# Performance work log

Hardware: AMD Instinct MI355X
Metric: run time of the kernel (lower is better)

The kernel has to match this reference:

```python
import jax, jax.numpy as jnp
import numpy as np

D, V, B, T = 512, 32000, 64, 32


def setup_inputs() -> dict:
    key = jax.random.key(0)
    ks = jax.random.split(key, 12)
    s = 1.0 / np.sqrt(D)
    u = lambda k, shape: jax.random.uniform(k, shape, jnp.float32, -s, s)
    return {
        "feats": jax.random.normal(ks[0], (B, D), jnp.float32),
        "W_ih": u(ks[1], (4 * D, D)),
        "W_hh": u(ks[2], (4 * D, D)),
        "b_ih": u(ks[3], (4 * D,)),
        "b_hh": u(ks[4], (4 * D,)),
        "W_hc": u(ks[5], (D, 2 * D)),
        "b_hc": u(ks[6], (D,)),
        "ln_gamma": jnp.ones((D,), jnp.float32),
        "ln_beta": jnp.zeros((D,), jnp.float32),
        "vocab_emb": jax.random.normal(ks[7], (V, D), jnp.float32),
        "vocab_bias": jnp.zeros((V,), jnp.float32),
        "max_seq_len": T,
    }


def reference(feats, W_ih, W_hh, b_ih, b_hh, W_hc, b_hc, ln_gamma, ln_beta,
              vocab_emb, vocab_bias, max_seq_len):
    b, d = feats.shape

    def cell(x, h, c):
        # torch.nn.LSTMCell: gate order i, f, g, o
        g = x @ W_ih.T + b_ih + h @ W_hh.T + b_hh  # [B, 4D]
        i, f, gg, o = jnp.split(g, 4, axis=-1)
        c2 = jax.nn.sigmoid(f) * c + jax.nn.sigmoid(i) * jnp.tanh(gg)
        h2 = jax.nn.sigmoid(o) * jnp.tanh(c2)
        return h2, c2

    def ln(x):
        m = x.mean(-1, keepdims=True)
        v = x.var(-1, keepdims=True)
        return (x - m) / jnp.sqrt(v + 1e-5) * ln_gamma + ln_beta

    emb0 = jnp.broadcast_to(vocab_emb[0], (b, d))  # vocab_encoder(zeros)

    def step(carry, _):
        h, c, emb = carry
        h, c = cell(emb, h, c)
        # outer-product attention: scores[b,i,j] = feats[b,i] * h[b,j]
        scores = feats[:, :, None] * h[:, None, :]  # [B, D, D]
        a = jax.nn.softmax(scores, axis=1)
        context = jnp.einsum('bij,bj->bi', a, feats)  # [B, D]
        z = jnp.concatenate([h, context], axis=-1) @ W_hc.T + b_hc
        emb = jnp.tanh(ln(z))
        logits = emb @ vocab_emb.T + vocab_bias  # [B, V]
        return (h, c, emb), logits

    _, logits = jax.lax.scan(step, (feats, feats, emb0), None, length=max_seq_len)
    return logits  # [T, B, V]
```

## Files before the change

kernel.cpp:

```cpp
#include <hip/hip_runtime.h>

#define DD 512
#define BB 64
#define VV 32000
#define TT 32

typedef __attribute__((ext_vector_type(8))) short short8;
typedef __attribute__((ext_vector_type(4))) float f32x4;
typedef __attribute__((ext_vector_type(4))) unsigned short ushort4v;

__device__ __forceinline__ float sigm(float x) { return 1.0f / (1.0f + __expf(-x)); }
__device__ __forceinline__ float ftanh(float x) {
  float e = __expf(2.0f * x);
  return 1.0f - 2.0f / (e + 1.0f);
}
__device__ __forceinline__ unsigned short f2bf(float f) {
  unsigned int u = __float_as_uint(f);
  u = (u + 0x7FFFu + ((u >> 16) & 1u)) >> 16;
  return (unsigned short)u;
}

__global__ __launch_bounds__(256) void prep_vocab_k(const float* __restrict__ v,
                                                    unsigned short* __restrict__ o) {
  size_t i = (size_t)blockIdx.x * 256 + threadIdx.x;
  float4 x = ((const float4*)v)[i];
  ushort4v y;
  y.x = f2bf(x.x); y.y = f2bf(x.y); y.z = f2bf(x.z); y.w = f2bf(x.w);
  ((ushort4v*)o)[i] = y;
}

__global__ __launch_bounds__(256) void init_k(const float* __restrict__ feats,
                                              const float* __restrict__ vocab,
                                              float* __restrict__ h, float* __restrict__ c,
                                              float* __restrict__ emb) {
  int i = blockIdx.x * 256 + threadIdx.x;
  float f = feats[i];
  h[i] = f; c[i] = f;
  emb[i] = vocab[i & 511];
}

__global__ __launch_bounds__(256) void cell_k(const float* __restrict__ Wih, const float* __restrict__ Whh,
    const float* __restrict__ bih, const float* __restrict__ bhh,
    const float* __restrict__ emb, const float* __restrict__ h_old, const float* __restrict__ c_old,
    float* __restrict__ h_new, float* __restrict__ c_new)
{
  __shared__ float4 xs4[16][128];
  __shared__ float4 hs4[16][128];
  __shared__ float gv[8][4][16];
  int tid = threadIdx.x;
  int bg = blockIdx.x >> 6, cg = blockIdx.x & 63;
  int b0 = bg * 16, d0 = cg * 8;
  const float4* ep = (const float4*)emb;
  const float4* hp = (const float4*)h_old;
  for (int i = tid; i < 2048; i += 256) {
    int b = i >> 7, k4 = i & 127;
    xs4[b][k4] = ep[(size_t)(b0 + b) * 128 + k4];
    hs4[b][k4] = hp[(size_t)(b0 + b) * 128 + k4];
  }
  __syncthreads();
  int rl = tid & 31, dl = rl >> 2, gate = rl & 3, bl = tid >> 5;
  int r = gate * 512 + d0 + dl;
  const float4* wi = (const float4*)(Wih + (size_t)r * 512);
  const float4* wh = (const float4*)(Whh + (size_t)r * 512);
  float acc0 = 0.f, acc1 = 0.f;
#pragma unroll 4
  for (int k4 = 0; k4 < 128; k4++) {
    float4 a = wi[k4], w = wh[k4];
    float4 x0 = xs4[bl][k4], x1 = xs4[bl + 8][k4];
    float4 h0 = hs4[bl][k4], h1 = hs4[bl + 8][k4];
    acc0 = fmaf(a.x, x0.x, acc0); acc0 = fmaf(a.y, x0.y, acc0);
    acc0 = fmaf(a.z, x0.z, acc0); acc0 = fmaf(a.w, x0.w, acc0);
    acc0 = fmaf(w.x, h0.x, acc0); acc0 = fmaf(w.y, h0.y, acc0);
    acc0 = fmaf(w.z, h0.z, acc0); acc0 = fmaf(w.w, h0.w, acc0);
    acc1 = fmaf(a.x, x1.x, acc1); acc1 = fmaf(a.y, x1.y, acc1);
    acc1 = fmaf(a.z, x1.z, acc1); acc1 = fmaf(a.w, x1.w, acc1);
    acc1 = fmaf(w.x, h1.x, acc1); acc1 = fmaf(w.y, h1.y, acc1);
    acc1 = fmaf(w.z, h1.z, acc1); acc1 = fmaf(w.w, h1.w, acc1);
  }
  float bias = bih[r] + bhh[r];
  gv[dl][gate][bl] = acc0 + bias;
  gv[dl][gate][bl + 8] = acc1 + bias;
  __syncthreads();
  if (tid < 128) {
    int b = tid & 15, dx = tid >> 4;
    float gi = gv[dx][0][b], gf = gv[dx][1][b], gg = gv[dx][2][b], go = gv[dx][3][b];
    size_t idx = (size_t)(b0 + b) * 512 + d0 + dx;
    float c2 = sigm(gf) * c_old[idx] + sigm(gi) * ftanh(gg);
    c_new[idx] = c2;
    h_new[idx] = sigm(go) * ftanh(c2);
  }
}

__global__ __launch_bounds__(512) void attnZ_k(const float* __restrict__ feats,
    const float* __restrict__ h, float* __restrict__ Zpart)
{
  int b = blockIdx.x >> 2, iq = blockIdx.x & 3;
  int tid = threadIdx.x;
  __shared__ float fs[128];
  if (tid < 128) fs[tid] = feats[b * 512 + iq * 128 + tid];
  __syncthreads();
  float hj = h[b * 512 + tid];
  float p = 0.f;
#pragma unroll 8
  for (int ii = 0; ii < 128; ii++) p += __expf(fs[ii] * hj);
  Zpart[(size_t)(iq * 64 + b) * 512 + tid] = p;
}

__global__ __launch_bounds__(512) void attnC_k(const float* __restrict__ feats,
    const float* __restrict__ h, const float* __restrict__ Zpart, float* __restrict__ ctxp)
{
  int b = blockIdx.x >> 2, jq = blockIdx.x & 3;
  int tid = threadIdx.x;
  __shared__ float hw[128], ww[128];
  if (tid < 128) {
    int j = jq * 128 + tid;
    float Z = Zpart[(size_t)(0 * 64 + b) * 512 + j] + Zpart[(size_t)(1 * 64 + b) * 512 + j]
            + Zpart[(size_t)(2 * 64 + b) * 512 + j] + Zpart[(size_t)(3 * 64 + b) * 512 + j];
    hw[tid] = h[b * 512 + j];
    ww[tid] = feats[b * 512 + j] / Z;
  }
  __syncthreads();
  float fi = feats[b * 512 + tid];
  float p = 0.f;
#pragma unroll 8
  for (int jj = 0; jj < 128; jj++) p += __expf(fi * hw[jj]) * ww[jj];
  ctxp[(size_t)(jq * 64 + b) * 512 + tid] = p;
}

__global__ __launch_bounds__(256) void zgemm_k(const float* __restrict__ h,
    const float* __restrict__ ctxp, const float* __restrict__ Whc, const float* __restrict__ bhc,
    float* __restrict__ z)
{
  __shared__ float4 hs4[16][128];
  __shared__ float4 cs4[16][128];
  __shared__ float zp[2][16][8];
  int tid = threadIdx.x;
  int bg = blockIdx.x >> 6, cg = blockIdx.x & 63;
  int b0 = bg * 16, d0 = cg * 8;
  const float4* hp = (const float4*)h;
  const float4* cp = (const float4*)ctxp;
  for (int i = tid; i < 2048; i += 256) {
    int b = i >> 7, k4 = i & 127;
    hs4[b][k4] = hp[(size_t)(b0 + b) * 128 + k4];
    float4 s0 = cp[(size_t)(0 * 64 + b0 + b) * 128 + k4];
    float4 s1 = cp[(size_t)(1 * 64 + b0 + b) * 128 + k4];
    float4 s2 = cp[(size_t)(2 * 64 + b0 + b) * 128 + k4];
    float4 s3 = cp[(size_t)(3 * 64 + b0 + b) * 128 + k4];
    float4 s; s.x = s0.x+s1.x+s2.x+s3.x; s.y = s0.y+s1.y+s2.y+s3.y;
    s.z = s0.z+s1.z+s2.z+s3.z; s.w = s0.w+s1.w+s2.w+s3.w;
    cs4[b][k4] = s;
  }
  __syncthreads();
  int dl = tid & 7, b = (tid >> 3) & 15, kh = tid >> 7;
  int dcol = d0 + dl;
  const float4* wr = (const float4*)(Whc + (size_t)dcol * 1024 + (size_t)kh * 512);
  float4 (*src)[128] = kh ? cs4 : hs4;
  float acc = 0.f;
#pragma unroll 4
  for (int k4 = 0; k4 < 128; k4++) {
    float4 w = wr[k4], x = src[b][k4];
    acc = fmaf(w.x, x.x, acc); acc = fmaf(w.y, x.y, acc);
    acc = fmaf(w.z, x.z, acc); acc = fmaf(w.w, x.w, acc);
  }
  zp[kh][b][dl] = acc;
  __syncthreads();
  if (tid < 128) {
    int bb = tid >> 3, dd = tid & 7;
    z[(size_t)(b0 + bb) * 512 + d0 + dd] = zp[0][bb][dd] + zp[1][bb][dd] + bhc[d0 + dd];
  }
}

__global__ __launch_bounds__(256) void ln_k(const float* __restrict__ z, const float* __restrict__ gamma,
    const float* __restrict__ beta, float* __restrict__ emb, unsigned short* __restrict__ emb_bf)
{
  int b = blockIdx.x, tid = threadIdx.x;
  __shared__ float zs[512];
  __shared__ float rs[256], rq[256];
  float a = z[b * 512 + tid], d = z[b * 512 + 256 + tid];
  zs[tid] = a; zs[tid + 256] = d;
  rs[tid] = a + d; rq[tid] = a * a + d * d;
  __syncthreads();
  for (int s = 128; s > 0; s >>= 1) {
    if (tid < s) { rs[tid] += rs[tid + s]; rq[tid] += rq[tid + s]; }
    __syncthreads();
  }
  float mean = rs[0] * (1.0f / 512.0f);
  float var = rq[0] * (1.0f / 512.0f) - mean * mean;
  float rstd = rsqrtf(var + 1e-5f);
  for (int d2 = tid; d2 < 512; d2 += 256) {
    float xn = (zs[d2] - mean) * rstd;
    float e = ftanh(xn * gamma[d2] + beta[d2]);
    emb[b * 512 + d2] = e;
    emb_bf[b * 512 + d2] = f2bf(e);
  }
}

__global__ __launch_bounds__(256) void logits_k(const unsigned short* __restrict__ emb_bf,
    const unsigned short* __restrict__ vocab_bf, const float* __restrict__ vbias,
    float* __restrict__ out)
{
  int n0 = blockIdx.x * 64;
  int w = threadIdx.x >> 6, l = threadIdx.x & 63;
  int lm = l & 15, kb = l >> 4;
  int m = w * 16 + lm;
  f32x4 acc[4] = {};
  const short8* ap = (const short8*)(emb_bf + (size_t)m * 512);
  for (int kt = 0; kt < 16; kt++) {
    short8 a = ap[kt * 4 + kb];
#pragma unroll
    for (int nt = 0; nt < 4; nt++) {
      const short8* bp = (const short8*)(vocab_bf + (size_t)(n0 + nt * 16 + lm) * 512);
      short8 bv = bp[kt * 4 + kb];
      acc[nt] = __builtin_amdgcn_mfma_f32_16x16x32_bf16(a, bv, acc[nt], 0, 0, 0);
    }
  }
  int rbase = w * 16 + kb * 4;
#pragma unroll
  for (int nt = 0; nt < 4; nt++) {
    int v = n0 + nt * 16 + lm;
    float bias = vbias[v];
#pragma unroll
    for (int r = 0; r < 4; r++) {
      out[(size_t)(rbase + r) * 32000 + v] = acc[nt][r] + bias;
    }
  }
}

extern "C" void kernel_launch(void* const* d_in, const int* in_sizes, int n_in,
                              void* d_out, int out_size, void* d_ws, size_t ws_size,
                              hipStream_t stream) {
  const float* feats = (const float*)d_in[0];
  const float* Wih  = (const float*)d_in[1];
  const float* Whh  = (const float*)d_in[2];
  const float* bih  = (const float*)d_in[3];
  const float* bhh  = (const float*)d_in[4];
  const float* Whc  = (const float*)d_in[5];
  const float* bhc  = (const float*)d_in[6];
  const float* gam  = (const float*)d_in[7];
  const float* bet  = (const float*)d_in[8];
  const float* vemb = (const float*)d_in[9];
  const float* vbias= (const float*)d_in[10];
  float* out = (float*)d_out;

  char* p = (char*)d_ws;
  unsigned short* vocab_bf = (unsigned short*)p; p += (size_t)VV * DD * 2;
  float* hA  = (float*)p; p += BB * DD * 4;
  float* hB  = (float*)p; p += BB * DD * 4;
  float* cA  = (float*)p; p += BB * DD * 4;
  float* cB  = (float*)p; p += BB * DD * 4;
  float* emb = (float*)p; p += BB * DD * 4;
  float* zb  = (float*)p; p += BB * DD * 4;
  unsigned short* emb_bf = (unsigned short*)p; p += BB * DD * 2;
  float* Zpart = (float*)p; p += (size_t)4 * BB * DD * 4;
  float* ctxp  = (float*)p; p += (size_t)4 * BB * DD * 4;

  prep_vocab_k<<<16000, 256, 0, stream>>>(vemb, vocab_bf);
  init_k<<<128, 256, 0, stream>>>(feats, vemb, hA, cA, emb);

  for (int t = 0; t < TT; t++) {
    float* ho = (t & 1) ? hB : hA; float* hn = (t & 1) ? hA : hB;
    float* co = (t & 1) ? cB : cA; float* cn = (t & 1) ? cA : cB;
    cell_k<<<256, 256, 0, stream>>>(Wih, Whh, bih, bhh, emb, ho, co, hn, cn);
    attnZ_k<<<256, 512, 0, stream>>>(feats, hn, Zpart);
    attnC_k<<<256, 512, 0, stream>>>(feats, hn, Zpart, ctxp);
    zgemm_k<<<256, 256, 0, stream>>>(hn, ctxp, Whc, bhc, zb);
    ln_k<<<64, 256, 0, stream>>>(zb, gam, bet, emb, emb_bf);
    logits_k<<<500, 256, 0, stream>>>(emb_bf, vocab_bf, vbias, out + (size_t)t * BB * VV);
  }
}
```

Baseline: 2.762 ms.

## Fuse all timesteps into one persistent kernel with grid barriers and overlapped logits

```diff
diff --git a/kernel.cpp b/kernel.cpp
--- a/kernel.cpp
+++ b/kernel.cpp
@@ -4,6 +4,9 @@
 #define BB 64
 #define VV 32000
 #define TT 32
+#define GRID 256
+#define NTHR 256
+#define NTILE 500
 
 typedef __attribute__((ext_vector_type(8))) short short8;
 typedef __attribute__((ext_vector_type(4))) float f32x4;
@@ -20,42 +23,49 @@
   return (unsigned short)u;
 }
 
-__global__ __launch_bounds__(256) void prep_vocab_k(const float* __restrict__ v,
-                                                    unsigned short* __restrict__ o) {
-  size_t i = (size_t)blockIdx.x * 256 + threadIdx.x;
-  float4 x = ((const float4*)v)[i];
-  ushort4v y;
-  y.x = f2bf(x.x); y.y = f2bf(x.y); y.z = f2bf(x.z); y.w = f2bf(x.w);
-  ((ushort4v*)o)[i] = y;
-}
-
-__global__ __launch_bounds__(256) void init_k(const float* __restrict__ feats,
-                                              const float* __restrict__ vocab,
-                                              float* __restrict__ h, float* __restrict__ c,
-                                              float* __restrict__ emb) {
-  int i = blockIdx.x * 256 + threadIdx.x;
-  float f = feats[i];
-  h[i] = f; c[i] = f;
-  emb[i] = vocab[i & 511];
-}
-
-__global__ __launch_bounds__(256) void cell_k(const float* __restrict__ Wih, const float* __restrict__ Whh,
+struct CellS { float4 xs4[16][128]; float4 hs4[16][128]; float gv[8][4][16]; };
+struct AttnS { float fsc[512]; float hs[512]; float wv[256]; };
+struct ZS    { float4 hs4[16][128]; float4 cs4[16][128]; float zp[2][16][8]; };
+struct LnS   { float zs[512]; float rs[256]; float rq[256]; };
+
+__device__ __forceinline__ void gridsync(unsigned* bar) {
+  __syncthreads();
+  if (threadIdx.x == 0) {
+    __threadfence();
+    unsigned* cnt = bar;
+    unsigned* gen = bar + 32;
+    unsigned g = __hip_atomic_load(gen, __ATOMIC_RELAXED, __HIP_MEMORY_SCOPE_AGENT);
+    unsigned old = __hip_atomic_fetch_add(cnt, 1u, __ATOMIC_ACQ_REL, __HIP_MEMORY_SCOPE_AGENT);
+    if (old == GRID - 1) {
+      __hip_atomic_store(cnt, 0u, __ATOMIC_RELAXED, __HIP_MEMORY_SCOPE_AGENT);
+      __hip_atomic_fetch_add(gen, 1u, __ATOMIC_ACQ_REL, __HIP_MEMORY_SCOPE_AGENT);
+    } else {
+      while (__hip_atomic_load(gen, __ATOMIC_ACQUIRE, __HIP_MEMORY_SCOPE_AGENT) == g)
+        __builtin_amdgcn_s_sleep(2);
+    }
+    __threadfence();
+  }
+  __syncthreads();
+}
+
+__global__ void bar_init_k(unsigned* bar) { bar[threadIdx.x] = 0u; }
+
+__device__ __forceinline__ void cell_phase(char* smemraw, int bid,
+    const float* __restrict__ Wih, const float* __restrict__ Whh,
     const float* __restrict__ bih, const float* __restrict__ bhh,
-    const float* __restrict__ emb, const float* __restrict__ h_old, const float* __restrict__ c_old,
-    float* __restrict__ h_new, float* __restrict__ c_new)
-{
-  __shared__ float4 xs4[16][128];
-  __shared__ float4 hs4[16][128];
-  __shared__ float gv[8][4][16];
+    const float* __restrict__ emb, const float* __restrict__ h_old,
+    const float* __restrict__ c_old, float* __restrict__ h_new, float* __restrict__ c_new)
+{
+  CellS& S = *reinterpret_cast<CellS*>(smemraw);
   int tid = threadIdx.x;
-  int bg = blockIdx.x >> 6, cg = blockIdx.x & 63;
+  int bg = bid >> 6, cg = bid & 63;
   int b0 = bg * 16, d0 = cg * 8;
   const float4* ep = (const float4*)emb;
   const float4* hp = (const float4*)h_old;
   for (int i = tid; i < 2048; i += 256) {
     int b = i >> 7, k4 = i & 127;
-    xs4[b][k4] = ep[(size_t)(b0 + b) * 128 + k4];
-    hs4[b][k4] = hp[(size_t)(b0 + b) * 128 + k4];
+    S.xs4[b][k4] = ep[(size_t)(b0 + b) * 128 + k4];
+    S.hs4[b][k4] = hp[(size_t)(b0 + b) * 128 + k4];
   }
   __syncthreads();
   int rl = tid & 31, dl = rl >> 2, gate = rl & 3, bl = tid >> 5;
@@ -66,8 +76,8 @@
 #pragma unroll 4
   for (int k4 = 0; k4 < 128; k4++) {
     float4 a = wi[k4], w = wh[k4];
-    float4 x0 = xs4[bl][k4], x1 = xs4[bl + 8][k4];
-    float4 h0 = hs4[bl][k4], h1 = hs4[bl + 8][k4];
+    float4 x0 = S.xs4[bl][k4], x1 = S.xs4[bl + 8][k4];
+    float4 h0 = S.hs4[bl][k4], h1 = S.hs4[bl + 8][k4];
     acc0 = fmaf(a.x, x0.x, acc0); acc0 = fmaf(a.y, x0.y, acc0);
     acc0 = fmaf(a.z, x0.z, acc0); acc0 = fmaf(a.w, x0.w, acc0);
     acc0 = fmaf(w.x, h0.x, acc0); acc0 = fmaf(w.y, h0.y, acc0);
@@ -78,12 +88,12 @@
     acc1 = fmaf(w.z, h1.z, acc1); acc1 = fmaf(w.w, h1.w, acc1);
   }
   float bias = bih[r] + bhh[r];
-  gv[dl][gate][bl] = acc0 + bias;
-  gv[dl][gate][bl + 8] = acc1 + bias;
+  S.gv[dl][gate][bl] = acc0 + bias;
+  S.gv[dl][gate][bl + 8] = acc1 + bias;
   __syncthreads();
   if (tid < 128) {
     int b = tid & 15, dx = tid >> 4;
-    float gi = gv[dx][0][b], gf = gv[dx][1][b], gg = gv[dx][2][b], go = gv[dx][3][b];
+    float gi = S.gv[dx][0][b], gf = S.gv[dx][1][b], gg = S.gv[dx][2][b], go = S.gv[dx][3][b];
     size_t idx = (size_t)(b0 + b) * 512 + d0 + dx;
     float c2 = sigm(gf) * c_old[idx] + sigm(gi) * ftanh(gg);
     c_new[idx] = c2;
@@ -91,70 +101,61 @@
   }
 }
 
-__global__ __launch_bounds__(512) void attnZ_k(const float* __restrict__ feats,
-    const float* __restrict__ h, float* __restrict__ Zpart)
-{
-  int b = blockIdx.x >> 2, iq = blockIdx.x & 3;
+__device__ __forceinline__ void attn_phase(char* smemraw, int bid,
+    const float* __restrict__ feats, const float* __restrict__ h, float* __restrict__ ctxp)
+{
+  AttnS& S = *reinterpret_cast<AttnS*>(smemraw);
   int tid = threadIdx.x;
-  __shared__ float fs[128];
-  if (tid < 128) fs[tid] = feats[b * 512 + iq * 128 + tid];
-  __syncthreads();
-  float hj = h[b * 512 + tid];
-  float p = 0.f;
+  int b = bid >> 1, jh = bid & 1;
+  const float LOG2E = 1.44269504088896f;
+  float f0 = feats[b * 512 + tid], f1 = feats[b * 512 + 256 + tid];
+  S.fsc[tid] = f0 * LOG2E;
+  S.fsc[256 + tid] = f1 * LOG2E;
+  S.hs[tid] = h[b * 512 + tid];
+  S.hs[256 + tid] = h[b * 512 + 256 + tid];
+  __syncthreads();
+  int j = jh * 256 + tid;
+  float hj = S.hs[j];
+  float Z = 0.f;
 #pragma unroll 8
-  for (int ii = 0; ii < 128; ii++) p += __expf(fs[ii] * hj);
-  Zpart[(size_t)(iq * 64 + b) * 512 + tid] = p;
-}
-
-__global__ __launch_bounds__(512) void attnC_k(const float* __restrict__ feats,
-    const float* __restrict__ h, const float* __restrict__ Zpart, float* __restrict__ ctxp)
-{
-  int b = blockIdx.x >> 2, jq = blockIdx.x & 3;
+  for (int i = 0; i < 512; i++) Z += exp2f(S.fsc[i] * hj);
+  S.wv[tid] = feats[b * 512 + j] / Z;
+  __syncthreads();
+#pragma unroll
+  for (int rep = 0; rep < 2; rep++) {
+    int i = rep * 256 + tid;
+    float fi = S.fsc[i];
+    float acc = 0.f;
+#pragma unroll 8
+    for (int jj = 0; jj < 256; jj++)
+      acc += exp2f(fi * S.hs[jh * 256 + jj]) * S.wv[jj];
+    ctxp[((size_t)jh * 64 + b) * 512 + i] = acc;
+  }
+}
+
+__device__ __forceinline__ void zgemm_phase(char* smemraw, int bid,
+    const float* __restrict__ h, const float* __restrict__ ctxp,
+    const float* __restrict__ Whc, const float* __restrict__ bhc, float* __restrict__ z)
+{
+  ZS& S = *reinterpret_cast<ZS*>(smemraw);
   int tid = threadIdx.x;
-  __shared__ float hw[128], ww[128];
-  if (tid < 128) {
-    int j = jq * 128 + tid;
-    float Z = Zpart[(size_t)(0 * 64 + b) * 512 + j] + Zpart[(size_t)(1 * 64 + b) * 512 + j]
-            + Zpart[(size_t)(2 * 64 + b) * 512 + j] + Zpart[(size_t)(3 * 64 + b) * 512 + j];
-    hw[tid] = h[b * 512 + j];
-    ww[tid] = feats[b * 512 + j] / Z;
-  }
-  __syncthreads();
-  float fi = feats[b * 512 + tid];
-  float p = 0.f;
-#pragma unroll 8
-  for (int jj = 0; jj < 128; jj++) p += __expf(fi * hw[jj]) * ww[jj];
-  ctxp[(size_t)(jq * 64 + b) * 512 + tid] = p;
-}
-
-__global__ __launch_bounds__(256) void zgemm_k(const float* __restrict__ h,
-    const float* __restrict__ ctxp, const float* __restrict__ Whc, const float* __restrict__ bhc,
-    float* __restrict__ z)
-{
-  __shared__ float4 hs4[16][128];
-  __shared__ float4 cs4[16][128];
-  __shared__ float zp[2][16][8];
-  int tid = threadIdx.x;
-  int bg = blockIdx.x >> 6, cg = blockIdx.x & 63;
+  int bg = bid >> 6, cg = bid & 63;
   int b0 = bg * 16, d0 = cg * 8;
   const float4* hp = (const float4*)h;
   const float4* cp = (const float4*)ctxp;
   for (int i = tid; i < 2048; i += 256) {
     int b = i >> 7, k4 = i & 127;
-    hs4[b][k4] = hp[(size_t)(b0 + b) * 128 + k4];
-    float4 s0 = cp[(size_t)(0 * 64 + b0 + b) * 128 + k4];
-    float4 s1 = cp[(size_t)(1 * 64 + b0 + b) * 128 + k4];
-    float4 s2 = cp[(size_t)(2 * 64 + b0 + b) * 128 + k4];
-    float4 s3 = cp[(size_t)(3 * 64 + b0 + b) * 128 + k4];
-    float4 s; s.x = s0.x+s1.x+s2.x+s3.x; s.y = s0.y+s1.y+s2.y+s3.y;
-    s.z = s0.z+s1.z+s2.z+s3.z; s.w = s0.w+s1.w+s2.w+s3.w;
-    cs4[b][k4] = s;
+    S.hs4[b][k4] = hp[(size_t)(b0 + b) * 128 + k4];
+    float4 s0 = cp[((size_t)0 * 64 + b0 + b) * 128 + k4];
+    float4 s1 = cp[((size_t)1 * 64 + b0 + b) * 128 + k4];
+    float4 s; s.x = s0.x + s1.x; s.y = s0.y + s1.y; s.z = s0.z + s1.z; s.w = s0.w + s1.w;
+    S.cs4[b][k4] = s;
   }
   __syncthreads();
   int dl = tid & 7, b = (tid >> 3) & 15, kh = tid >> 7;
   int dcol = d0 + dl;
   const float4* wr = (const float4*)(Whc + (size_t)dcol * 1024 + (size_t)kh * 512);
-  float4 (*src)[128] = kh ? cs4 : hs4;
+  float4 (*src)[128] = kh ? S.cs4 : S.hs4;
   float acc = 0.f;
 #pragma unroll 4
   for (int k4 = 0; k4 < 128; k4++) {
@@ -162,49 +163,51 @@
     acc = fmaf(w.x, x.x, acc); acc = fmaf(w.y, x.y, acc);
     acc = fmaf(w.z, x.z, acc); acc = fmaf(w.w, x.w, acc);
   }
-  zp[kh][b][dl] = acc;
+  S.zp[kh][b][dl] = acc;
   __syncthreads();
   if (tid < 128) {
     int bb = tid >> 3, dd = tid & 7;
-    z[(size_t)(b0 + bb) * 512 + d0 + dd] = zp[0][bb][dd] + zp[1][bb][dd] + bhc[d0 + dd];
-  }
-}
-
-__global__ __launch_bounds__(256) void ln_k(const float* __restrict__ z, const float* __restrict__ gamma,
-    const float* __restrict__ beta, float* __restrict__ emb, unsigned short* __restrict__ emb_bf)
-{
-  int b = blockIdx.x, tid = threadIdx.x;
-  __shared__ float zs[512];
-  __shared__ float rs[256], rq[256];
+    z[(size_t)(b0 + bb) * 512 + d0 + dd] = S.zp[0][bb][dd] + S.zp[1][bb][dd] + bhc[d0 + dd];
+  }
+}
+
+__device__ __forceinline__ void ln_phase(char* smemraw, int b,
+    const float* __restrict__ z, const float* __restrict__ gamma, const float* __restrict__ beta,
+    float* __restrict__ emb, unsigned short* __restrict__ emb_bf)
+{
+  LnS& S = *reinterpret_cast<LnS*>(smemraw);
+  int tid = threadIdx.x;
   float a = z[b * 512 + tid], d = z[b * 512 + 256 + tid];
-  zs[tid] = a; zs[tid + 256] = d;
-  rs[tid] = a + d; rq[tid] = a * a + d * d;
+  S.zs[tid] = a; S.zs[tid + 256] = d;
+  S.rs[tid] = a + d; S.rq[tid] = a * a + d * d;
   __syncthreads();
   for (int s = 128; s > 0; s >>= 1) {
-    if (tid < s) { rs[tid] += rs[tid + s]; rq[tid] += rq[tid + s]; }
+    if (tid < s) { S.rs[tid] += S.rs[tid + s]; S.rq[tid] += S.rq[tid + s]; }
     __syncthreads();
   }
-  float mean = rs[0] * (1.0f / 512.0f);
-  float var = rq[0] * (1.0f / 512.0f) - mean * mean;
+  float mean = S.rs[0] * (1.0f / 512.0f);
+  float var = S.rq[0] * (1.0f / 512.0f) - mean * mean;
   float rstd = rsqrtf(var + 1e-5f);
   for (int d2 = tid; d2 < 512; d2 += 256) {
-    float xn = (zs[d2] - mean) * rstd;
+    float xn = (S.zs[d2] - mean) * rstd;
     float e = ftanh(xn * gamma[d2] + beta[d2]);
     emb[b * 512 + d2] = e;
     emb_bf[b * 512 + d2] = f2bf(e);
   }
 }
 
-__global__ __launch_bounds__(256) void logits_k(const unsigned short* __restrict__ emb_bf,
+__device__ __forceinline__ void logits_tile(const unsigned short* __restrict__ emb_bf,
     const unsigned short* __restrict__ vocab_bf, const float* __restrict__ vbias,
-    float* __restrict__ out)
-{
-  int n0 = blockIdx.x * 64;
+    float* __restrict__ out, int q)
+{
+  if (q >= NTILE) return;
+  int n0 = q * 64;
   int w = threadIdx.x >> 6, l = threadIdx.x & 63;
   int lm = l & 15, kb = l >> 4;
   int m = w * 16 + lm;
   f32x4 acc[4] = {};
   const short8* ap = (const short8*)(emb_bf + (size_t)m * 512);
+#pragma unroll 4
   for (int kt = 0; kt < 16; kt++) {
     short8 a = ap[kt * 4 + kb];
 #pragma unroll
@@ -226,20 +229,93 @@
   }
 }
 
+__global__ __launch_bounds__(256, 1) void persist_k(
+    const float* __restrict__ feats, const float* __restrict__ Wih, const float* __restrict__ Whh,
+    const float* __restrict__ bih, const float* __restrict__ bhh,
+    const float* __restrict__ Whc, const float* __restrict__ bhc,
+    const float* __restrict__ gam, const float* __restrict__ bet,
+    const float* __restrict__ vemb, const float* __restrict__ vbias,
+    unsigned short* vocab_bf, float* hA, float* hB, float* cA, float* cB,
+    float* emb, float* zb, unsigned short* ebf0, unsigned short* ebf1,
+    float* ctxp, float* out, unsigned* bar)
+{
+  __shared__ __align__(16) char smem[sizeof(CellS)];
+  const int bid = blockIdx.x, tid = threadIdx.x;
+
+  {
+    const float4* vp = (const float4*)vemb;
+    ushort4v* op = (ushort4v*)vocab_bf;
+    for (int i = bid * NTHR + tid; i < VV * DD / 4; i += GRID * NTHR) {
+      float4 x = vp[i];
+      ushort4v y;
+      y.x = f2bf(x.x); y.y = f2bf(x.y); y.z = f2bf(x.z); y.w = f2bf(x.w);
+      op[i] = y;
+    }
+    for (int i = bid * NTHR + tid; i < BB * DD; i += GRID * NTHR) {
+      float f = feats[i];
+      hA[i] = f; cA[i] = f;
+      emb[i] = vemb[i & (DD - 1)];
+    }
+  }
+  gridsync(bar);
+
+  for (int t = 0; t < TT; t++) {
+    float* ho = (t & 1) ? hB : hA; float* hn = (t & 1) ? hA : hB;
+    float* co = (t & 1) ? cB : cA; float* cn = (t & 1) ? cA : cB;
+    unsigned short* ebf_cur  = (t & 1) ? ebf1 : ebf0;
+    unsigned short* ebf_prev = (t & 1) ? ebf0 : ebf1;
+    float* out_prev = out + (size_t)(t - 1) * BB * VV;
+
+    cell_phase(smem, bid, Wih, Whh, bih, bhh, emb, ho, co, hn, cn);
+    gridsync(bar);
+
+    if (bid < 128) {
+      attn_phase(smem, bid, feats, hn, ctxp);
+    } else if (t >= 1) {
+      int idx = bid - 128;
+      logits_tile(ebf_prev, vocab_bf, vbias, out_prev, idx * 2);
+      logits_tile(ebf_prev, vocab_bf, vbias, out_prev, idx * 2 + 1);
+    }
+    gridsync(bar);
+
+    zgemm_phase(smem, bid, hn, ctxp, Whc, bhc, zb);
+    gridsync(bar);
+
+    if (bid < 64) {
+      ln_phase(smem, bid, zb, gam, bet, emb, ebf_cur);
+    } else if (t >= 1) {
+      int idx = bid - 64;
+      if (idx < 52) {
+        logits_tile(ebf_prev, vocab_bf, vbias, out_prev, 256 + 2 * idx);
+        logits_tile(ebf_prev, vocab_bf, vbias, out_prev, 257 + 2 * idx);
+      } else {
+        logits_tile(ebf_prev, vocab_bf, vbias, out_prev, 360 + (idx - 52));
+      }
+    }
+    gridsync(bar);
+  }
+
+  {
+    float* o31 = out + (size_t)(TT - 1) * BB * VV;
+    logits_tile(ebf1, vocab_bf, vbias, o31, bid * 2);
+    logits_tile(ebf1, vocab_bf, vbias, o31, bid * 2 + 1);
+  }
+}
+
 extern "C" void kernel_launch(void* const* d_in, const int* in_sizes, int n_in,
                               void* d_out, int out_size, void* d_ws, size_t ws_size,
                               hipStream_t stream) {
   const float* feats = (const float*)d_in[0];
-  const float* Wih  = (const float*)d_in[1];
-  const float* Whh  = (const float*)d_in[2];
-  const float* bih  = (const float*)d_in[3];
-  const float* bhh  = (const float*)d_in[4];
-  const float* Whc  = (const float*)d_in[5];
-  const float* bhc  = (const float*)d_in[6];
-  const float* gam  = (const float*)d_in[7];
-  const float* bet  = (const float*)d_in[8];
-  const float* vemb = (const float*)d_in[9];
-  const float* vbias= (const float*)d_in[10];
+  const float* Wih   = (const float*)d_in[1];
+  const float* Whh   = (const float*)d_in[2];
+  const float* bih   = (const float*)d_in[3];
+  const float* bhh   = (const float*)d_in[4];
+  const float* Whc   = (const float*)d_in[5];
+  const float* bhc   = (const float*)d_in[6];
+  const float* gam   = (const float*)d_in[7];
+  const float* bet   = (const float*)d_in[8];
+  const float* vemb  = (const float*)d_in[9];
+  const float* vbias = (const float*)d_in[10];
   float* out = (float*)d_out;
 
   char* p = (char*)d_ws;
@@ -250,21 +326,13 @@
   float* cB  = (float*)p; p += BB * DD * 4;
   float* emb = (float*)p; p += BB * DD * 4;
   float* zb  = (float*)p; p += BB * DD * 4;
-  unsigned short* emb_bf = (unsigned short*)p; p += BB * DD * 2;
-  float* Zpart = (float*)p; p += (size_t)4 * BB * DD * 4;
-  float* ctxp  = (float*)p; p += (size_t)4 * BB * DD * 4;
-
-  prep_vocab_k<<<16000, 256, 0, stream>>>(vemb, vocab_bf);
-  init_k<<<128, 256, 0, stream>>>(feats, vemb, hA, cA, emb);
-
-  for (int t = 0; t < TT; t++) {
-    float* ho = (t & 1) ? hB : hA; float* hn = (t & 1) ? hA : hB;
-    float* co = (t & 1) ? cB : cA; float* cn = (t & 1) ? cA : cB;
-    cell_k<<<256, 256, 0, stream>>>(Wih, Whh, bih, bhh, emb, ho, co, hn, cn);
-    attnZ_k<<<256, 512, 0, stream>>>(feats, hn, Zpart);
-    attnC_k<<<256, 512, 0, stream>>>(feats, hn, Zpart, ctxp);
-    zgemm_k<<<256, 256, 0, stream>>>(hn, ctxp, Whc, bhc, zb);
-    ln_k<<<64, 256, 0, stream>>>(zb, gam, bet, emb, emb_bf);
-    logits_k<<<500, 256, 0, stream>>>(emb_bf, vocab_bf, vbias, out + (size_t)t * BB * VV);
-  }
-}
+  unsigned short* ebf0 = (unsigned short*)p; p += BB * DD * 2;
+  unsigned short* ebf1 = (unsigned short*)p; p += BB * DD * 2;
+  float* ctxp = (float*)p; p += (size_t)2 * BB * DD * 4;
+  unsigned* bar = (unsigned*)p; p += 256;
+
+  bar_init_k<<<1, 64, 0, stream>>>(bar);
+  persist_k<<<GRID, NTHR, 0, stream>>>(feats, Wih, Whh, bih, bhh, Whc, bhc, gam, bet,
+                                       vemb, vbias, vocab_bf, hA, hB, cA, cB, emb, zb,
+                                       ebf0, ebf1, ctxp, out, bar);
+}
```

Result: slower. 6.607 ms (+139.2%).
